# Kernel optimization log

Hardware: AMD Instinct MI355X
Metric: run time of the kernel (lower is better)

## Reference

```python
import jax, jax.numpy as jnp
import numpy as np


def conv2d(x, w, b):
    # x: [B,C,H,W], w: [O,C,K,K] (VALID, stride 1)
    out = jax.lax.conv_general_dilated(
        x, w, window_strides=(1, 1), padding='VALID',
        dimension_numbers=('NCHW', 'OIHW', 'NCHW'))
    return out + b[None, :, None, None]


def deform_conv2d(x, offset, w, b):
    # torchvision DeformConv2d semantics, offset_groups=1, stride=1, padding=0.
    # x: [B,C,H,W]; offset: [B, 2*K*K, Ho, Wo] with (dy, dx) interleaved per tap.
    B, C, H, W = x.shape
    O, _, K, _ = w.shape
    KK = K * K
    Ho, Wo = H - K + 1, W - K + 1
    off = offset.reshape(B, KK, 2, Ho, Wo)
    ky = (jnp.arange(KK) // K).astype(x.dtype)
    kx = (jnp.arange(KK) % K).astype(x.dtype)
    # sampling positions p0 + p_k + dp  -> [B, KK, Ho, Wo]
    py = ky[None, :, None, None] + jnp.arange(Ho, dtype=x.dtype)[None, None, :, None] + off[:, :, 0]
    px = kx[None, :, None, None] + jnp.arange(Wo, dtype=x.dtype)[None, None, None, :] + off[:, :, 1]
    y0 = jnp.floor(py)
    x0 = jnp.floor(px)
    wy = py - y0  # fractional parts
    wx = px - x0
    y0i = y0.astype(jnp.int32)
    x0i = x0.astype(jnp.int32)

    def corner(yi, xi):
        valid = ((yi >= 0) & (yi < H) & (xi >= 0) & (xi < W)).astype(x.dtype)
        yc = jnp.clip(yi, 0, H - 1)
        xc = jnp.clip(xi, 0, W - 1)
        # per-batch gather over all channels -> [B, C, KK, Ho, Wo]
        g = jax.vmap(lambda im, a, bb: im[:, a, bb])(x, yc, xc)
        return g * valid[:, None]

    v00 = corner(y0i, x0i)
    v01 = corner(y0i, x0i + 1)
    v10 = corner(y0i + 1, x0i)
    v11 = corner(y0i + 1, x0i + 1)
    wy_ = wy[:, None]  # [B,1,KK,Ho,Wo]
    wx_ = wx[:, None]
    samp = (v00 * (1 - wy_) * (1 - wx_) + v01 * (1 - wy_) * wx_
            + v10 * wy_ * (1 - wx_) + v11 * wy_ * wx_)
    out = jnp.einsum('bckhw,ock->bohw', samp, w.reshape(O, C, KK))
    return out + b[None, :, None, None]


_STAGES = [
    # (in_ch, out_ch, K)
    (1, 16, 3), (16, 32, 3), (32, 16, 5), (16, 16, 7), (16, 8, 5), (8, 4, 3),
]


def setup_inputs() -> dict:
    key = jax.random.key(0)
    keys = iter(jax.random.split(key, 64))
    inp = {'x': jax.random.normal(next(keys), (512, 1, 33, 33), dtype=jnp.float32)}
    for i, (ci, co, k) in enumerate(_STAGES, start=1):
        # offset-predicting conv: small init so offsets stay near the regular grid
        inp[f'ow{i}'] = jax.random.normal(next(keys), (2 * k * k, ci, k, k), dtype=jnp.float32) * 0.05
        inp[f'ob{i}'] = jax.random.normal(next(keys), (2 * k * k,), dtype=jnp.float32) * 0.05
        scale = 1.0 / np.sqrt(ci * k * k)
        inp[f'w{i}'] = jax.random.normal(next(keys), (co, ci, k, k), dtype=jnp.float32) * scale
        inp[f'b{i}'] = jax.random.normal(next(keys), (co,), dtype=jnp.float32) * scale
    inp['fc1_w'] = jax.random.normal(next(keys), (256, 13 * 13 * 4), dtype=jnp.float32) * (1.0 / np.sqrt(676))
    inp['fc1_b'] = jnp.zeros((256,), dtype=jnp.float32)
    inp['fc2_w'] = jax.random.normal(next(keys), (10, 256), dtype=jnp.float32) * (1.0 / np.sqrt(256))
    inp['fc2_b'] = jnp.zeros((10,), dtype=jnp.float32)
    return inp


def reference(x, ow1, ob1, w1, b1, ow2, ob2, w2, b2, ow3, ob3, w3, b3,
              ow4, ob4, w4, b4, ow5, ob5, w5, b5, ow6, ob6, w6, b6,
              fc1_w, fc1_b, fc2_w, fc2_b):
    h = jax.nn.relu(deform_conv2d(x, conv2d(x, ow1, ob1), w1, b1))
    h = jax.nn.relu(deform_conv2d(h, conv2d(h, ow2, ob2), w2, b2))
    h = deform_conv2d(h, conv2d(h, ow3, ob3), w3, b3)  # NOTE: no ReLU on stage 3 (matches source)
    h = jax.nn.relu(deform_conv2d(h, conv2d(h, ow4, ob4), w4, b4))
    h = jax.nn.relu(deform_conv2d(h, conv2d(h, ow5, ob5), w5, b5))
    h = jax.nn.relu(deform_conv2d(h, conv2d(h, ow6, ob6), w6, b6))
    flat = h.reshape(h.shape[0], -1)  # [B, 4*13*13]
    z = jax.nn.relu(flat @ fc1_w.T + fc1_b)
    return z @ fc2_w.T + fc2_b
```

## Files before the change

kernel.cpp:

```cpp
#include <hip/hip_runtime.h>

typedef __attribute__((ext_vector_type(8))) short bf16x8;
typedef __attribute__((ext_vector_type(4))) float f32x4;
typedef __attribute__((ext_vector_type(4))) unsigned int u32x4;
typedef unsigned short ushort_t;

__device__ inline ushort_t bf16_trunc(float f) { return (ushort_t)(__float_as_uint(f) >> 16); }
__device__ inline float bf16_to_f(ushort_t u) { return __uint_as_float(((unsigned int)u) << 16); }

__device__ inline unsigned int hi_pair(unsigned int u1, unsigned int u0) {
    return __builtin_amdgcn_perm(u1, u0, 0x07060302u);
}

__device__ inline void split8(const f32x4 sA, const f32x4 sB, bf16x8& ahi, bf16x8& alo)
{
    unsigned int u[8], h[8], d[8];
#pragma unroll
    for (int j = 0; j < 4; ++j) {
        u[j]     = __float_as_uint(sA[j]);
        u[4 + j] = __float_as_uint(sB[j]);
    }
#pragma unroll
    for (int j = 0; j < 8; ++j) {
        h[j] = u[j] & 0xffff0000u;
        d[j] = __float_as_uint(__uint_as_float(u[j]) - __uint_as_float(h[j]));
    }
    union { u32x4 w; bf16x8 v; } H, L;
    H.w = (u32x4){hi_pair(h[1], h[0]), hi_pair(h[3], h[2]), hi_pair(h[5], h[4]), hi_pair(h[7], h[6])};
    L.w = (u32x4){hi_pair(d[1], d[0]), hi_pair(d[3], d[2]), hi_pair(d[5], d[4]), hi_pair(d[7], d[6])};
    ahi = H.v;
    alo = L.v;
}

template<int CI, int KK, int KKPAD, int NPAD, int OC>
__global__ __launch_bounds__(256)
void wprep(const float* __restrict__ w, ushort_t* __restrict__ bhi, ushort_t* __restrict__ blo)
{
    const int idx = blockIdx.x * 256 + threadIdx.x;
    if (idx >= KKPAD * NPAD * CI) return;
    const int kk  = idx / (NPAD * CI);
    const int rem = idx - kk * (NPAD * CI);
    const int n   = rem / CI;
    const int ci  = rem - n * CI;
    const float v = (kk < KK && n < OC) ? w[((size_t)n * CI + ci) * KK + kk] : 0.f;
    const ushort_t h = bf16_trunc(v);
    bhi[idx] = h;
    blo[idx] = bf16_trunc(v - bf16_to_f(h));
}

template<int CI, int KK, int TPAD, int NPAD, int OC>
__global__ __launch_bounds__(256)
void wprep_d(const float* __restrict__ w, ushort_t* __restrict__ bhi, ushort_t* __restrict__ blo)
{
    constexpr int NPASS = (CI + 7) / 8;
    constexpr int TOTAL = NPASS * TPAD * NPAD * 8;
    const int idx = blockIdx.x * 256 + threadIdx.x;
    if (idx >= TOTAL) return;
    const int j     = idx & 7;
    const int n     = (idx >> 3) % NPAD;
    const int kslot = (idx >> 3) / NPAD;
    const int pass  = kslot / TPAD;
    const int tap   = kslot - pass * TPAD;
    const int ci    = pass * 8 + j;
    const float v = (tap < KK && n < OC && ci < CI) ? w[((size_t)n * CI + ci) * KK + tap] : 0.f;
    const ushort_t h = bf16_trunc(v);
    bhi[idx] = h;
    blo[idx] = bf16_trunc(v - bf16_to_f(h));
}

template<int CI, int K, int H, int W, int Ho, int Wo, int OC, int NTTOT, int NT0, int KSTEPS>
__global__ __launch_bounds__(256)
void conv_mfma(const ushort_t* __restrict__ Xhi, const ushort_t* __restrict__ Xlo,
               const ushort_t* __restrict__ Bhi, const ushort_t* __restrict__ Blo,
               const float* __restrict__ bias, float* __restrict__ out, int Mtotal)
{
    constexpr int NPAD = NTTOT * 16;
    constexpr int HW   = H * W;
    constexpr int HoWo = Ho * Wo;
    constexpr int NPASS = CI / 8;
    constexpr int TKS  = 32 / CI;
    constexpr int ROWS = TKS * NT0 * 16;
    constexpr int BSTR = CI + 8;
    constexpr int CH8  = CI / 8;
    constexpr int CHUNKS = ROWS * CH8;

    __shared__ __align__(16) ushort_t sBh[2][ROWS * BSTR];
    __shared__ __align__(16) ushort_t sBl[2][ROWS * BSTR];

    const int tid  = threadIdx.x;
    const int lane = tid & 63;
    const int wid  = tid >> 6;
    const int col  = lane & 15;
    const int quad = lane >> 4;

    const int mBase  = blockIdx.x * 256 + wid * 64;
    const int ntBase = blockIdx.y * NT0;

    int aBase[4];
#pragma unroll
    for (int mt = 0; mt < 4; ++mt) {
        int mm = mBase + mt * 16 + col;
        if (mm >= Mtotal) mm = Mtotal - 1;
        const int b   = mm / HoWo;
        const int pos = mm - b * HoWo;
        const int oy  = pos / Wo;
        const int ox  = pos - oy * Wo;
        aBase[mt] = b * NPASS * HW + oy * W + ox;
    }

    f32x4 acc[4][NT0];
#pragma unroll
    for (int mt = 0; mt < 4; ++mt)
#pragma unroll
        for (int nt = 0; nt < NT0; ++nt) acc[mt][nt] = (f32x4){0.f, 0.f, 0.f, 0.f};

    auto loadSlab = [&](int ks, int buf) {
        const int tap0 = ks * TKS;
        for (int i = tid; i < CHUNKS; i += 256) {
            const int row = i / CH8;
            const int c8  = i - row * CH8;
            const int t   = row / (NT0 * 16);
            const int nn  = row - t * (NT0 * 16);
            int n = ntBase * 16 + nn;
            if (n > NPAD - 1) n = NPAD - 1;
            const int g = ((tap0 + t) * NPAD + n) * CI + c8 * 8;
            *(bf16x8*)(sBh[buf] + row * BSTR + c8 * 8) = *(const bf16x8*)(Bhi + g);
            *(bf16x8*)(sBl[buf] + row * BSTR + c8 * 8) = *(const bf16x8*)(Blo + g);
        }
    };

    bf16x8 ah[2][4], al[2][4];

    auto loadA = [&](int ks, int pb) {
        const int k0   = ks * 32 + quad * 8;
        const int tap  = k0 / CI;
        const int ci   = k0 - tap * CI;
        const int g    = ci >> 3;
        const int dkk  = (tap / K) * W + (tap - (tap / K) * K);
#pragma unroll
        for (int mt = 0; mt < 4; ++mt) {
            const size_t aoff = (size_t)(aBase[mt] + g * HW + dkk) * 8;
            ah[pb][mt] = *(const bf16x8*)(Xhi + aoff);
            al[pb][mt] = *(const bf16x8*)(Xlo + aoff);
        }
    };

    loadA(0, 0);
    loadSlab(0, 0);
    __syncthreads();

#pragma unroll
    for (int ks = 0; ks < KSTEPS; ++ks) {
        if (ks + 1 < KSTEPS) {
            loadA(ks + 1, (ks + 1) & 1);
            loadSlab(ks + 1, (ks + 1) & 1);
        }

        const int k0   = ks * 32 + quad * 8;
        const int tap  = k0 / CI;
        const int tloc = tap - ks * TKS;
        const int ci   = k0 - tap * CI;
        const int pb   = ks & 1;

        const ushort_t* __restrict__ bhp = sBh[pb];
        const ushort_t* __restrict__ blp = sBl[pb];
#pragma unroll
        for (int nt = 0; nt < NT0; ++nt) {
            const int ntg = ntBase + nt;
            if (ntg < NTTOT) {
                const int lrow = ((tloc * NT0 + nt) * 16 + col) * BSTR + ci;
                const bf16x8 bh = *(const bf16x8*)(bhp + lrow);
                const bf16x8 bl = *(const bf16x8*)(blp + lrow);
#pragma unroll
                for (int mt = 0; mt < 4; ++mt) {
                    acc[mt][nt] = __builtin_amdgcn_mfma_f32_16x16x32_bf16(ah[pb][mt], bh, acc[mt][nt], 0, 0, 0);
                    acc[mt][nt] = __builtin_amdgcn_mfma_f32_16x16x32_bf16(al[pb][mt], bh, acc[mt][nt], 0, 0, 0);
                    acc[mt][nt] = __builtin_amdgcn_mfma_f32_16x16x32_bf16(ah[pb][mt], bl, acc[mt][nt], 0, 0, 0);
                }
            }
        }
        __syncthreads();
    }

#pragma unroll
    for (int mt = 0; mt < 4; ++mt) {
#pragma unroll
        for (int nt = 0; nt < NT0; ++nt) {
            const int ntg = ntBase + nt;
            const int n   = ntg * 16 + col;
            if (ntg < NTTOT && n < OC) {
                const float bv = bias[n];
#pragma unroll
                for (int r = 0; r < 4; ++r) {
                    const int m = mBase + mt * 16 + quad * 4 + r;
                    if (m < Mtotal) {
                        const int b   = m / HoWo;
                        const int pos = m - b * HoWo;
                        out[((size_t)b * OC + n) * HoWo + pos] = acc[mt][nt][r] + bv;
                    }
                }
            }
        }
    }
}

template<int K, int CI, int CO, int H, int W, int Ho, int Wo, bool RELU,
         int MT, int TPAD, bool OUTPL>
__global__ __launch_bounds__(MT * 64, 4)
void deform_mfma(const ushort_t* __restrict__ Xhi, const ushort_t* __restrict__ Xlo,
                 const float* __restrict__ off,
                 const ushort_t* __restrict__ Bph, const ushort_t* __restrict__ Bpl,
                 const float* __restrict__ bias,
                 float* __restrict__ outF, ushort_t* __restrict__ oHi, ushort_t* __restrict__ oLo)
{
    static_assert(CI % 8 == 0, "channel-grouped layout requires CI % 8 == 0");
    constexpr int KK     = K * K;
    constexpr int HW     = H * W;
    constexpr int HoWo   = Ho * Wo;
    constexpr int GP     = CI / 8;
    constexpr int NPO    = CO / 8;
    constexpr int NT     = (CO + 15) / 16;
    constexpr int NPAD   = NT * 16;
    constexpr int TSTR   = CI + 4;
    constexpr int TG     = TPAD / 4;
    constexpr int nMB    = (HoWo + MT * 16 - 1) / (MT * 16);
    constexpr int THREADS = MT * 64;
    __shared__ __align__(16) float tile[HW * TSTR];

    const int b    = blockIdx.x / nMB;
    const int mb   = blockIdx.x - b * nMB;
    const int tid  = threadIdx.x;
    const int wid  = tid >> 6;
    const int lane = tid & 63;
    const int col  = lane & 15;
    const int quad = lane >> 4;

    const int pixel0 = (mb * MT + wid) * 16;
    const int s      = pixel0 + col;
    const bool am    = (s < HoWo);
    const int oy = s / Wo, ox = s - oy * Wo;

    const float* offB = off + (size_t)b * 2 * KK * HoWo;

    f32x4 acc[NT];
#pragma unroll
    for (int nt = 0; nt < NT; ++nt) acc[nt] = (f32x4){0.f, 0.f, 0.f, 0.f};

    for (int pos = tid; pos < HW; pos += THREADS) {
        float* tp = tile + pos * TSTR;
#pragma unroll
        for (int g = 0; g < GP; ++g) {
            const size_t gbase = ((size_t)(b * GP + g) * HW + pos) * 8;
            const bf16x8 h8 = *(const bf16x8*)(Xhi + gbase);
            const bf16x8 l8 = *(const bf16x8*)(Xlo + gbase);
            f32x4 vA, vB;
#pragma unroll
            for (int j = 0; j < 4; ++j) {
                vA[j] = bf16_to_f((ushort_t)h8[j])     + bf16_to_f((ushort_t)l8[j]);
                vB[j] = bf16_to_f((ushort_t)h8[4 + j]) + bf16_to_f((ushort_t)l8[4 + j]);
            }
            *(f32x4*)(tp + g * 8)     = vA;
            *(f32x4*)(tp + g * 8 + 4) = vB;
        }
    }
    __syncthreads();

#pragma unroll
    for (int tg = 0; tg < TG; ++tg) {
        const int tap = tg * 4 + quad;

        float w00 = 0.f, w01 = 0.f, w10 = 0.f, w11 = 0.f;
        int   i00 = 0,   i01 = 0,   i10 = 0,   i11 = 0;

        if (am && tap < KK) {
            const float dy = offB[(size_t)(2 * tap + 0) * HoWo + s];
            const float dx = offB[(size_t)(2 * tap + 1) * HoWo + s];
            const float py = (float)(tap / K + oy) + dy;
            const float px = (float)(tap % K + ox) + dx;
            const float y0f = floorf(py), x0f = floorf(px);
            const float wy = py - y0f, wx = px - x0f;
            const int y0 = (int)y0f, x0 = (int)x0f;
            const int y1 = y0 + 1,   x1 = x0 + 1;

            const float m00 = (y0 >= 0 && y0 < H && x0 >= 0 && x0 < W) ? 1.f : 0.f;
            const float m01 = (y0 >= 0 && y0 < H && x1 >= 0 && x1 < W) ? 1.f : 0.f;
            const float m10 = (y1 >= 0 && y1 < H && x0 >= 0 && x0 < W) ? 1.f : 0.f;
            const float m11 = (y1 >= 0 && y1 < H && x1 >= 0 && x1 < W) ? 1.f : 0.f;

            w00 = (1.f - wy) * (1.f - wx) * m00;
            w01 = (1.f - wy) * wx         * m01;
            w10 = wy         * (1.f - wx) * m10;
            w11 = wy         * wx         * m11;

            const int y0c = min(max(y0, 0), H - 1), y1c = min(max(y1, 0), H - 1);
            const int x0c = min(max(x0, 0), W - 1), x1c = min(max(x1, 0), W - 1);
            i00 = (y0c * W + x0c) * TSTR;
            i01 = (y0c * W + x1c) * TSTR;
            i10 = (y1c * W + x0c) * TSTR;
            i11 = (y1c * W + x1c) * TSTR;
        }

#pragma unroll
        for (int g = 0; g < GP; ++g) {
            const float* tp = tile + g * 8;
            const f32x4 a00 = *(const f32x4*)(tp + i00);
            const f32x4 c00 = *(const f32x4*)(tp + i00 + 4);
            const f32x4 a01 = *(const f32x4*)(tp + i01);
            const f32x4 c01 = *(const f32x4*)(tp + i01 + 4);
            const f32x4 a10 = *(const f32x4*)(tp + i10);
            const f32x4 c10 = *(const f32x4*)(tp + i10 + 4);
            const f32x4 a11 = *(const f32x4*)(tp + i11);
            const f32x4 c11 = *(const f32x4*)(tp + i11 + 4);

            f32x4 sA = a00 * w00 + a01 * w01 + a10 * w10 + a11 * w11;
            f32x4 sB = c00 * w00 + c01 * w01 + c10 * w10 + c11 * w11;

            bf16x8 ahi, alo;
            split8(sA, sB, ahi, alo);

            const int kslot = g * TPAD + tap;
#pragma unroll
            for (int nt = 0; nt < NT; ++nt) {
                const bf16x8 bh = *(const bf16x8*)(Bph + ((size_t)kslot * NPAD + nt * 16 + col) * 8);
                const bf16x8 bl = *(const bf16x8*)(Bpl + ((size_t)kslot * NPAD + nt * 16 + col) * 8);
                acc[nt] = __builtin_amdgcn_mfma_f32_16x16x32_bf16(ahi, bh, acc[nt], 0, 0, 0);
                acc[nt] = __builtin_amdgcn_mfma_f32_16x16x32_bf16(alo, bh, acc[nt], 0, 0, 0);
                acc[nt] = __builtin_amdgcn_mfma_f32_16x16x32_bf16(ahi, bl, acc[nt], 0, 0, 0);
            }
        }
    }

#pragma unroll
    for (int nt = 0; nt < NT; ++nt) {
        const int n = nt * 16 + col;
        if (n < CO) {
            const float bv = bias[n];
#pragma unroll
            for (int r = 0; r < 4; ++r) {
                const int m = pixel0 + quad * 4 + r;
                if (m < HoWo) {
                    float v = acc[nt][r] + bv;
                    if (RELU) v = fmaxf(v, 0.f);
                    if (OUTPL) {
                        const size_t o = (((size_t)b * NPO + (n >> 3)) * HoWo + m) * 8 + (n & 7);
                        const ushort_t h = bf16_trunc(v);
                        oHi[o] = h;
                        oLo[o] = bf16_trunc(v - bf16_to_f(h));
                    } else {
                        outF[((size_t)b * CO + n) * HoWo + m] = v;
                    }
                }
            }
        }
    }
}

template<int K, int CI, int CO, int H, int W, int Ho, int Wo, bool RELU,
         int CSPLIT, int STRIDE, int THREADS, int SPLIT, bool OUTPL>
__global__ __launch_bounds__(THREADS)
void deform_lds(const float* __restrict__ x, const float* __restrict__ off,
                const float* __restrict__ w, const float* __restrict__ bias,
                float* __restrict__ outF, ushort_t* __restrict__ oHi, ushort_t* __restrict__ oLo)
{
    constexpr int KK    = K * K;
    constexpr int HW    = H * W;
    constexpr int HoWo  = Ho * Wo;
    constexpr int NPASS = CI / CSPLIT;
    constexpr int NPO   = (CO + 7) / 8;
    constexpr int CHUNK = (HoWo + SPLIT - 1) / SPLIT;
    static_assert(CHUNK <= THREADS, "chunk must fit in one block");
    __shared__ __align__(16) float tile[HW * STRIDE];

    const int b   = blockIdx.x / SPLIT;
    const int sp  = blockIdx.x - b * SPLIT;
    const int tid = threadIdx.x;
    const int s   = sp * CHUNK + tid;
    const bool active = (tid < CHUNK) && (s < HoWo);

    const int oy = s / Wo, ox = s - oy * Wo;
    const float* offp = off + ((size_t)b * 2 * KK) * HoWo + s;

    float acc[CO];
#pragma unroll
    for (int o = 0; o < CO; ++o) acc[o] = 0.f;

    for (int pass = 0; pass < NPASS; ++pass) {
        const int cbase = pass * CSPLIT;
        __syncthreads();
        for (int pos = tid; pos < HW; pos += THREADS) {
#pragma unroll
            for (int c = 0; c < CSPLIT; ++c)
                tile[pos * STRIDE + c] = x[((size_t)b * CI + (cbase + c)) * HW + pos];
        }
        __syncthreads();

        if (active) {
            for (int kk = 0; kk < KK; ++kk) {
                const float dy = offp[(size_t)(2 * kk + 0) * HoWo];
                const float dx = offp[(size_t)(2 * kk + 1) * HoWo];
                const float py = (float)(kk / K + oy) + dy;
                const float px = (float)(kk % K + ox) + dx;
                const float y0f = floorf(py), x0f = floorf(px);
                const float wy = py - y0f, wx = px - x0f;
                const int y0 = (int)y0f, x0 = (int)x0f;
                const int y1 = y0 + 1,   x1 = x0 + 1;

                const float m00 = (y0 >= 0 && y0 < H && x0 >= 0 && x0 < W) ? 1.f : 0.f;
                const float m01 = (y0 >= 0 && y0 < H && x1 >= 0 && x1 < W) ? 1.f : 0.f;
                const float m10 = (y1 >= 0 && y1 < H && x0 >= 0 && x0 < W) ? 1.f : 0.f;
                const float m11 = (y1 >= 0 && y1 < H && x1 >= 0 && x1 < W) ? 1.f : 0.f;

                const float w00 = (1.f - wy) * (1.f - wx) * m00;
                const float w01 = (1.f - wy) * wx         * m01;
                const float w10 = wy         * (1.f - wx) * m10;
                const float w11 = wy         * wx         * m11;

                const int y0c = min(max(y0, 0), H - 1), y1c = min(max(y1, 0), H - 1);
                const int x0c = min(max(x0, 0), W - 1), x1c = min(max(x1, 0), W - 1);
                const int i00 = (y0c * W + x0c) * STRIDE;
                const int i01 = (y0c * W + x1c) * STRIDE;
                const int i10 = (y1c * W + x0c) * STRIDE;
                const int i11 = (y1c * W + x1c) * STRIDE;

                if constexpr (CSPLIT % 4 == 0) {
#pragma unroll
                    for (int cg = 0; cg < CSPLIT; cg += 4) {
                        const f32x4 v00 = *(const f32x4*)(tile + i00 + cg);
                        const f32x4 v01 = *(const f32x4*)(tile + i01 + cg);
                        const f32x4 v10 = *(const f32x4*)(tile + i10 + cg);
                        const f32x4 v11 = *(const f32x4*)(tile + i11 + cg);
#pragma unroll
                        for (int j = 0; j < 4; ++j) {
                            const float sv = fmaf(v11[j], w11, fmaf(v10[j], w10,
                                             fmaf(v01[j], w01, v00[j] * w00)));
#pragma unroll
                            for (int o = 0; o < CO; ++o)
                                acc[o] = fmaf(sv, w[(size_t)(o * CI + cbase + cg + j) * KK + kk], acc[o]);
                        }
                    }
                } else {
                    const float sv = fmaf(tile[i11], w11, fmaf(tile[i10], w10,
                                     fmaf(tile[i01], w01, tile[i00] * w00)));
#pragma unroll
                    for (int o = 0; o < CO; ++o)
                        acc[o] = fmaf(sv, w[(size_t)(o * CI + cbase) * KK + kk], acc[o]);
                }
            }
        }
    }

    if (active) {
#pragma unroll
        for (int o = 0; o < CO; ++o) {
            float v = acc[o] + bias[o];
            if (RELU) v = fmaxf(v, 0.f);
            if (OUTPL) {
                const size_t oi = (((size_t)b * NPO + (o >> 3)) * HoWo + s) * 8 + (o & 7);
                const ushort_t h = bf16_trunc(v);
                oHi[oi] = h;
                oLo[oi] = bf16_trunc(v - bf16_to_f(h));
            } else {
                outF[((size_t)b * CO + o) * HoWo + s] = v;
            }
        }
    }
}

template<int K, int CI, int NOC, int OC, int H, int W, int Ho, int Wo, int PIX>
__global__ __launch_bounds__(256)
void conv_tile(const float* __restrict__ x, const float* __restrict__ w,
               const float* __restrict__ bias, float* __restrict__ out)
{
    constexpr int KK   = K * K;
    constexpr int HoWo = Ho * Wo;
    constexpr int WoG  = (Wo + PIX - 1) / PIX;
    constexpr int G    = Ho * WoG;
    constexpr int XV   = PIX + K - 1;

    const int oc0   = blockIdx.y * NOC;
    const int g_all = blockIdx.x * 256 + threadIdx.x;
    const int b     = g_all / G;
    const int g     = g_all - b * G;
    const int oy    = g / WoG;
    const int ox0   = (g - oy * WoG) * PIX;

    const float* xbp = x + (b * CI) * (H * W) + oy * W + ox0;
    const float* wp  = w + oc0 * (CI * KK);

    float acc[PIX][NOC];
#pragma unroll
    for (int p = 0; p < PIX; ++p)
#pragma unroll
        for (int j = 0; j < NOC; ++j) acc[p][j] = bias[oc0 + j];

    const int lim = W - 1 - ox0;

    for (int ci = 0; ci < CI; ++ci) {
        const float* xc = xbp + ci * (H * W);
#pragma unroll
        for (int ky = 0; ky < K; ++ky) {
            float xv[XV];
#pragma unroll
            for (int i = 0; i < XV; ++i) {
                const int off = (i <= lim) ? i : lim;
                xv[i] = xc[ky * W + off];
            }
#pragma unroll
            for (int kx = 0; kx < K; ++kx) {
#pragma unroll
                for (int p = 0; p < PIX; ++p) {
                    const float v = xv[p + kx];
#pragma unroll
                    for (int j = 0; j < NOC; ++j)
                        acc[p][j] = fmaf(v, wp[j * (CI * KK) + ci * KK + ky * K + kx], acc[p][j]);
                }
            }
        }
    }

    float* op = out + (b * OC + oc0) * HoWo + oy * Wo + ox0;
#pragma unroll
    for (int p = 0; p < PIX; ++p) {
        if (ox0 + p < Wo) {
#pragma unroll
            for (int j = 0; j < NOC; ++j) op[j * HoWo + p] = acc[p][j];
        }
    }
}

template<int IN, int OUT>
__global__ __launch_bounds__(256)
void wtrans(const float* __restrict__ w, float* __restrict__ wt)
{
    const int idx = blockIdx.x * 256 + threadIdx.x;
    if (idx >= IN * OUT) return;
    const int i = idx / OUT, j = idx - i * OUT;
    wt[idx] = w[(size_t)j * IN + i];
}

template<int IN, int OUT, bool RELU>
__global__ __launch_bounds__(256)
void fc_t(const float* __restrict__ h, const float* __restrict__ wt,
          const float* __restrict__ bias, float* __restrict__ out, int B)
{
    const int idx = blockIdx.x * 256 + threadIdx.x;
    if (idx >= B * OUT) return;
    const int b = idx / OUT;
    const int j = idx - b * OUT;
    const float* hb = h + (size_t)b * IN;
    float acc = bias[j];
#pragma unroll 4
    for (int i = 0; i < IN; ++i)
        acc = fmaf(hb[i], wt[(size_t)i * OUT + j], acc);
    if (RELU) acc = fmaxf(acc, 0.f);
    out[idx] = acc;
}

extern "C" void kernel_launch(void* const* d_in, const int* in_sizes, int n_in,
                              void* d_out, int out_size, void* d_ws, size_t ws_size,
                              hipStream_t stream)
{
    const int B = 512;
    const float* x = (const float*)d_in[0];
    const float *ow[6], *ob[6], *w[6], *bi[6];
    for (int i = 0; i < 6; ++i) {
        ow[i] = (const float*)d_in[1 + 4 * i];
        ob[i] = (const float*)d_in[2 + 4 * i];
        w[i]  = (const float*)d_in[3 + 4 * i];
        bi[i] = (const float*)d_in[4 + 4 * i];
    }
    const float* fc1w = (const float*)d_in[25];
    const float* fc1b = (const float*)d_in[26];
    const float* fc2w = (const float*)d_in[27];
    const float* fc2b = (const float*)d_in[28];
    float* out = (float*)d_out;

    float* P   = (float*)d_ws;
    float* Q   = P  + 14000000;
    float* OFF = Q  + 14000000;
    float* Z   = OFF + 18200000;
    ushort_t* WBhi = (ushort_t*)(Z + 200000);
    ushort_t* WBlo = WBhi + 200000;
    ushort_t* WDhi = WBlo + 200000;
    ushort_t* WDlo = WDhi + 200000;
    float* WT1 = (float*)(WDlo + 200000);
    float* WT2 = WT1 + 173056;

    const dim3 blk(256);
    #define GRIDT(Ho, Wo, PIX, NG) dim3((B * (Ho) * (((Wo) + (PIX) - 1) / (PIX)) + 255) / 256, (NG), 1)
    #define CEILDIV(a, b) (((a) + (b) - 1) / (b))

    ushort_t* PL2h = (ushort_t*)Q;  ushort_t* PL2l = PL2h + (size_t)(B * 961 + 2048) * 16;
    ushort_t* PL3h = (ushort_t*)P;  ushort_t* PL3l = PL3h + (size_t)(B * 841 + 2048) * 32;
    ushort_t* PL4h = (ushort_t*)Q;  ushort_t* PL4l = PL4h + (size_t)(B * 625 + 2048) * 16;
    ushort_t* PL5h = (ushort_t*)P;  ushort_t* PL5l = PL5h + (size_t)(B * 361 + 2048) * 16;

    conv_tile<3, 1, 6, 18, 33, 33, 31, 31, 4><<<GRIDT(31, 31, 4, 3), blk, 0, stream>>>(x, ow[0], ob[0], OFF);
    deform_lds<3, 1, 16, 33, 33, 31, 31, true, 1, 1, 512, 2, true><<<dim3(B * 2), dim3(512), 0, stream>>>(x, OFF, w[0], bi[0], nullptr, PL2h, PL2l);

    {
        const int Mv = B * 841;
        wprep<16, 9, 10, 32, 18><<<CEILDIV(10 * 32 * 16, 256), blk, 0, stream>>>(ow[1], WBhi, WBlo);
        conv_mfma<16, 3, 31, 31, 29, 29, 18, 2, 2, 5><<<dim3(CEILDIV(Mv, 256), 1), blk, 0, stream>>>(PL2h, PL2l, WBhi, WBlo, ob[1], OFF, Mv);
        wprep_d<16, 9, 12, 32, 32><<<CEILDIV(2 * 12 * 32 * 8, 256), blk, 0, stream>>>(w[1], WDhi, WDlo);
        deform_mfma<3, 16, 32, 31, 31, 29, 29, true, 8, 12, true><<<dim3(B * 7), dim3(512), 0, stream>>>(PL2h, PL2l, OFF, WDhi, WDlo, bi[1], nullptr, PL3h, PL3l);
    }
    {
        const int Mv = B * 625;
        wprep<32, 25, 25, 64, 50><<<CEILDIV(25 * 64 * 32, 256), blk, 0, stream>>>(ow[2], WBhi, WBlo);
        conv_mfma<32, 5, 29, 29, 25, 25, 50, 4, 4, 25><<<dim3(CEILDIV(Mv, 256), 1), blk, 0, stream>>>(PL3h, PL3l, WBhi, WBlo, ob[2], OFF, Mv);
        wprep_d<32, 25, 28, 16, 16><<<CEILDIV(4 * 28 * 16 * 8, 256), blk, 0, stream>>>(w[2], WDhi, WDlo);
        deform_mfma<5, 32, 16, 29, 29, 25, 25, false, 14, 28, true><<<dim3(B * 3), dim3(896), 0, stream>>>(PL3h, PL3l, OFF, WDhi, WDlo, bi[2], nullptr, PL4h, PL4l);
    }
    {
        const int Mv = B * 361;
        wprep<16, 49, 50, 112, 98><<<CEILDIV(50 * 112 * 16, 256), blk, 0, stream>>>(ow[3], WBhi, WBlo);
        conv_mfma<16, 7, 25, 25, 19, 19, 98, 7, 4, 25><<<dim3(CEILDIV(Mv, 256), 2), blk, 0, stream>>>(PL4h, PL4l, WBhi, WBlo, ob[3], OFF, Mv);
        wprep_d<16, 49, 52, 16, 16><<<CEILDIV(2 * 52 * 16 * 8, 256), blk, 0, stream>>>(w[3], WDhi, WDlo);
        deform_mfma<7, 16, 16, 25, 25, 19, 19, true, 8, 52, true><<<dim3(B * 3), dim3(512), 0, stream>>>(PL4h, PL4l, OFF, WDhi, WDlo, bi[3], nullptr, PL5h, PL5l);
    }
    {
        const int Mv = B * 225;
        wprep<16, 25, 26, 64, 50><<<CEILDIV(26 * 64 * 16, 256), blk, 0, stream>>>(ow[4], WBhi, WBlo);
        conv_mfma<16, 5, 19, 19, 15, 15, 50, 4, 4, 13><<<dim3(CEILDIV(Mv, 256), 1), blk, 0, stream>>>(PL5h, PL5l, WBhi, WBlo, ob[4], OFF, Mv);
        wprep_d<16, 25, 28, 16, 8><<<CEILDIV(2 * 28 * 16 * 8, 256), blk, 0, stream>>>(w[4], WDhi, WDlo);
        deform_mfma<5, 16, 8, 19, 19, 15, 15, true, 4, 28, false><<<dim3(B * 4), dim3(256), 0, stream>>>(PL5h, PL5l, OFF, WDhi, WDlo, bi[4], Q, nullptr, nullptr);
    }
    conv_tile<3, 8, 6, 18, 15, 15, 13, 13, 4><<<GRIDT(13, 13, 4, 3), blk, 0, stream>>>(Q, ow[5], ob[5], OFF);
    deform_lds<3, 8, 4, 15, 15, 13, 13, true, 8, 12, 192, 1, false><<<dim3(B), dim3(192), 0, stream>>>(Q, OFF, w[5], bi[5], P, nullptr, nullptr);

    wtrans<676, 256><<<CEILDIV(676 * 256, 256), blk, 0, stream>>>(fc1w, WT1);
    wtrans<256, 10><<<CEILDIV(256 * 10, 256), blk, 0, stream>>>(fc2w, WT2);
    fc_t<676, 256, true><<<dim3(CEILDIV(B * 256, 256)), blk, 0, stream>>>(P, WT1, fc1b, Z, B);
    fc_t<256, 10, false><<<dim3(CEILDIV(B * 10, 256)), blk, 0, stream>>>(Z, WT2, fc2b, out, B);

    #undef GRIDT
    #undef CEILDIV
}
```

Baseline: 817.2 us.

## Use packed FP32 bilinear math, skip empty pixel tiles, enlarge deform blocks

The bilinear interpolation in deform_mfma now uses v_pk_mul_f32/v_pk_fma_f32 inline asm to process two channels per instruction. A guard skips the tap loop for waves whose pixel tile lies entirely outside the output. Three deform_mfma launches are retuned to use more waves per block and fewer blocks, so each block's LDS input tile serves more output pixels. The inline asm may limit compiler scheduling, and larger blocks can lower occupancy.

```diff
diff --git a/kernel.cpp b/kernel.cpp
--- a/kernel.cpp
+++ b/kernel.cpp
@@ -2,11 +2,23 @@
 
 typedef __attribute__((ext_vector_type(8))) short bf16x8;
 typedef __attribute__((ext_vector_type(4))) float f32x4;
+typedef __attribute__((ext_vector_type(2))) float f32x2;
 typedef __attribute__((ext_vector_type(4))) unsigned int u32x4;
 typedef unsigned short ushort_t;
 
 __device__ inline ushort_t bf16_trunc(float f) { return (ushort_t)(__float_as_uint(f) >> 16); }
 __device__ inline float bf16_to_f(ushort_t u) { return __uint_as_float(((unsigned int)u) << 16); }
+
+__device__ inline f32x2 pk_mul(f32x2 a, f32x2 b) {
+    f32x2 d;
+    asm("v_pk_mul_f32 %0, %1, %2" : "=v"(d) : "v"(a), "v"(b));
+    return d;
+}
+__device__ inline f32x2 pk_fma(f32x2 a, f32x2 b, f32x2 c) {
+    f32x2 d;
+    asm("v_pk_fma_f32 %0, %1, %2, %3" : "=v"(d) : "v"(a), "v"(b), "v"(c));
+    return d;
+}
 
 __device__ inline unsigned int hi_pair(unsigned int u1, unsigned int u0) {
     return __builtin_amdgcn_perm(u1, u0, 0x07060302u);
@@ -265,67 +277,92 @@
     }
     __syncthreads();
 
-#pragma unroll
-    for (int tg = 0; tg < TG; ++tg) {
-        const int tap = tg * 4 + quad;
-
-        float w00 = 0.f, w01 = 0.f, w10 = 0.f, w11 = 0.f;
-        int   i00 = 0,   i01 = 0,   i10 = 0,   i11 = 0;
-
-        if (am && tap < KK) {
-            const float dy = offB[(size_t)(2 * tap + 0) * HoWo + s];
-            const float dx = offB[(size_t)(2 * tap + 1) * HoWo + s];
-            const float py = (float)(tap / K + oy) + dy;
-            const float px = (float)(tap % K + ox) + dx;
-            const float y0f = floorf(py), x0f = floorf(px);
-            const float wy = py - y0f, wx = px - x0f;
-            const int y0 = (int)y0f, x0 = (int)x0f;
-            const int y1 = y0 + 1,   x1 = x0 + 1;
-
-            const float m00 = (y0 >= 0 && y0 < H && x0 >= 0 && x0 < W) ? 1.f : 0.f;
-            const float m01 = (y0 >= 0 && y0 < H && x1 >= 0 && x1 < W) ? 1.f : 0.f;
-            const float m10 = (y1 >= 0 && y1 < H && x0 >= 0 && x0 < W) ? 1.f : 0.f;
-            const float m11 = (y1 >= 0 && y1 < H && x1 >= 0 && x1 < W) ? 1.f : 0.f;
-
-            w00 = (1.f - wy) * (1.f - wx) * m00;
-            w01 = (1.f - wy) * wx         * m01;
-            w10 = wy         * (1.f - wx) * m10;
-            w11 = wy         * wx         * m11;
-
-            const int y0c = min(max(y0, 0), H - 1), y1c = min(max(y1, 0), H - 1);
-            const int x0c = min(max(x0, 0), W - 1), x1c = min(max(x1, 0), W - 1);
-            i00 = (y0c * W + x0c) * TSTR;
-            i01 = (y0c * W + x1c) * TSTR;
-            i10 = (y1c * W + x0c) * TSTR;
-            i11 = (y1c * W + x1c) * TSTR;
-        }
-
-#pragma unroll
-        for (int g = 0; g < GP; ++g) {
-            const float* tp = tile + g * 8;
-            const f32x4 a00 = *(const f32x4*)(tp + i00);
-            const f32x4 c00 = *(const f32x4*)(tp + i00 + 4);
-            const f32x4 a01 = *(const f32x4*)(tp + i01);
-            const f32x4 c01 = *(const f32x4*)(tp + i01 + 4);
-            const f32x4 a10 = *(const f32x4*)(tp + i10);
-            const f32x4 c10 = *(const f32x4*)(tp + i10 + 4);
-            const f32x4 a11 = *(const f32x4*)(tp + i11);
-            const f32x4 c11 = *(const f32x4*)(tp + i11 + 4);
-
-            f32x4 sA = a00 * w00 + a01 * w01 + a10 * w10 + a11 * w11;
-            f32x4 sB = c00 * w00 + c01 * w01 + c10 * w10 + c11 * w11;
-
-            bf16x8 ahi, alo;
-            split8(sA, sB, ahi, alo);
-
-            const int kslot = g * TPAD + tap;
-#pragma unroll
-            for (int nt = 0; nt < NT; ++nt) {
-                const bf16x8 bh = *(const bf16x8*)(Bph + ((size_t)kslot * NPAD + nt * 16 + col) * 8);
-                const bf16x8 bl = *(const bf16x8*)(Bpl + ((size_t)kslot * NPAD + nt * 16 + col) * 8);
-                acc[nt] = __builtin_amdgcn_mfma_f32_16x16x32_bf16(ahi, bh, acc[nt], 0, 0, 0);
-                acc[nt] = __builtin_amdgcn_mfma_f32_16x16x32_bf16(alo, bh, acc[nt], 0, 0, 0);
-                acc[nt] = __builtin_amdgcn_mfma_f32_16x16x32_bf16(ahi, bl, acc[nt], 0, 0, 0);
+    if (pixel0 < HoWo) {
+#pragma unroll
+        for (int tg = 0; tg < TG; ++tg) {
+            const int tap = tg * 4 + quad;
+
+            float w00 = 0.f, w01 = 0.f, w10 = 0.f, w11 = 0.f;
+            int   i00 = 0,   i01 = 0,   i10 = 0,   i11 = 0;
+
+            if (am && tap < KK) {
+                const float dy = offB[(size_t)(2 * tap + 0) * HoWo + s];
+                const float dx = offB[(size_t)(2 * tap + 1) * HoWo + s];
+                const float py = (float)(tap / K + oy) + dy;
+                const float px = (float)(tap % K + ox) + dx;
+                const float y0f = floorf(py), x0f = floorf(px);
+                const float wy = py - y0f, wx = px - x0f;
+                const int y0 = (int)y0f, x0 = (int)x0f;
+                const int y1 = y0 + 1,   x1 = x0 + 1;
+
+                const float m00 = (y0 >= 0 && y0 < H && x0 >= 0 && x0 < W) ? 1.f : 0.f;
+                const float m01 = (y0 >= 0 && y0 < H && x1 >= 0 && x1 < W) ? 1.f : 0.f;
+                const float m10 = (y1 >= 0 && y1 < H && x0 >= 0 && x0 < W) ? 1.f : 0.f;
+                const float m11 = (y1 >= 0 && y1 < H && x1 >= 0 && x1 < W) ? 1.f : 0.f;
+
+                w00 = (1.f - wy) * (1.f - wx) * m00;
+                w01 = (1.f - wy) * wx         * m01;
+                w10 = wy         * (1.f - wx) * m10;
+                w11 = wy         * wx         * m11;
+
+                const int y0c = min(max(y0, 0), H - 1), y1c = min(max(y1, 0), H - 1);
+                const int x0c = min(max(x0, 0), W - 1), x1c = min(max(x1, 0), W - 1);
+                i00 = (y0c * W + x0c) * TSTR;
+                i01 = (y0c * W + x1c) * TSTR;
+                i10 = (y1c * W + x0c) * TSTR;
+                i11 = (y1c * W + x1c) * TSTR;
+            }
+
+            const f32x2 w00p = {w00, w00}, w01p = {w01, w01};
+            const f32x2 w10p = {w10, w10}, w11p = {w11, w11};
+
+#pragma unroll
+            for (int g = 0; g < GP; ++g) {
+                const float* tp = tile + g * 8;
+                const f32x4 a00 = *(const f32x4*)(tp + i00);
+                const f32x4 c00 = *(const f32x4*)(tp + i00 + 4);
+                const f32x4 a01 = *(const f32x4*)(tp + i01);
+                const f32x4 c01 = *(const f32x4*)(tp + i01 + 4);
+                const f32x4 a10 = *(const f32x4*)(tp + i10);
+                const f32x4 c10 = *(const f32x4*)(tp + i10 + 4);
+                const f32x4 a11 = *(const f32x4*)(tp + i11);
+                const f32x4 c11 = *(const f32x4*)(tp + i11 + 4);
+
+#define LOH(v) __builtin_shufflevector(v, v, 0, 1)
+#define HIH(v) __builtin_shufflevector(v, v, 2, 3)
+                f32x2 sA0 = pk_mul(LOH(a00), w00p);
+                sA0 = pk_fma(LOH(a01), w01p, sA0);
+                sA0 = pk_fma(LOH(a10), w10p, sA0);
+                sA0 = pk_fma(LOH(a11), w11p, sA0);
+                f32x2 sA1 = pk_mul(HIH(a00), w00p);
+                sA1 = pk_fma(HIH(a01), w01p, sA1);
+                sA1 = pk_fma(HIH(a10), w10p, sA1);
+                sA1 = pk_fma(HIH(a11), w11p, sA1);
+                f32x2 sB0 = pk_mul(LOH(c00), w00p);
+                sB0 = pk_fma(LOH(c01), w01p, sB0);
+                sB0 = pk_fma(LOH(c10), w10p, sB0);
+                sB0 = pk_fma(LOH(c11), w11p, sB0);
+                f32x2 sB1 = pk_mul(HIH(c00), w00p);
+                sB1 = pk_fma(HIH(c01), w01p, sB1);
+                sB1 = pk_fma(HIH(c10), w10p, sB1);
+                sB1 = pk_fma(HIH(c11), w11p, sB1);
+#undef LOH
+#undef HIH
+                const f32x4 sA = __builtin_shufflevector(sA0, sA1, 0, 1, 2, 3);
+                const f32x4 sB = __builtin_shufflevector(sB0, sB1, 0, 1, 2, 3);
+
+                bf16x8 ahi, alo;
+                split8(sA, sB, ahi, alo);
+
+                const int kslot = g * TPAD + tap;
+#pragma unroll
+                for (int nt = 0; nt < NT; ++nt) {
+                    const bf16x8 bh = *(const bf16x8*)(Bph + ((size_t)kslot * NPAD + nt * 16 + col) * 8);
+                    const bf16x8 bl = *(const bf16x8*)(Bpl + ((size_t)kslot * NPAD + nt * 16 + col) * 8);
+                    acc[nt] = __builtin_amdgcn_mfma_f32_16x16x32_bf16(ahi, bh, acc[nt], 0, 0, 0);
+                    acc[nt] = __builtin_amdgcn_mfma_f32_16x16x32_bf16(alo, bh, acc[nt], 0, 0, 0);
+                    acc[nt] = __builtin_amdgcn_mfma_f32_16x16x32_bf16(ahi, bl, acc[nt], 0, 0, 0);
+                }
             }
         }
     }
@@ -603,7 +640,7 @@
         wprep<16, 9, 10, 32, 18><<<CEILDIV(10 * 32 * 16, 256), blk, 0, stream>>>(ow[1], WBhi, WBlo);
         conv_mfma<16, 3, 31, 31, 29, 29, 18, 2, 2, 5><<<dim3(CEILDIV(Mv, 256), 1), blk, 0, stream>>>(PL2h, PL2l, WBhi, WBlo, ob[1], OFF, Mv);
         wprep_d<16, 9, 12, 32, 32><<<CEILDIV(2 * 12 * 32 * 8, 256), blk, 0, stream>>>(w[1], WDhi, WDlo);
-        deform_mfma<3, 16, 32, 31, 31, 29, 29, true, 8, 12, true><<<dim3(B * 7), dim3(512), 0, stream>>>(PL2h, PL2l, OFF, WDhi, WDlo, bi[1], nullptr, PL3h, PL3l);
+        deform_mfma<3, 16, 32, 31, 31, 29, 29, true, 14, 12, true><<<dim3(B * 4), dim3(896), 0, stream>>>(PL2h, PL2l, OFF, WDhi, WDlo, bi[1], nullptr, PL3h, PL3l);
     }
     {
         const int Mv = B * 625;
@@ -617,14 +654,14 @@
         wprep<16, 49, 50, 112, 98><<<CEILDIV(50 * 112 * 16, 256), blk, 0, stream>>>(ow[3], WBhi, WBlo);
         conv_mfma<16, 7, 25, 25, 19, 19, 98, 7, 4, 25><<<dim3(CEILDIV(Mv, 256), 2), blk, 0, stream>>>(PL4h, PL4l, WBhi, WBlo, ob[3], OFF, Mv);
         wprep_d<16, 49, 52, 16, 16><<<CEILDIV(2 * 52 * 16 * 8, 256), blk, 0, stream>>>(w[3], WDhi, WDlo);
-        deform_mfma<7, 16, 16, 25, 25, 19, 19, true, 8, 52, true><<<dim3(B * 3), dim3(512), 0, stream>>>(PL4h, PL4l, OFF, WDhi, WDlo, bi[3], nullptr, PL5h, PL5l);
+        deform_mfma<7, 16, 16, 25, 25, 19, 19, true, 12, 52, true><<<dim3(B * 2), dim3(768), 0, stream>>>(PL4h, PL4l, OFF, WDhi, WDlo, bi[3], nullptr, PL5h, PL5l);
     }
     {
         const int Mv = B * 225;
         wprep<16, 25, 26, 64, 50><<<CEILDIV(26 * 64 * 16, 256), blk, 0, stream>>>(ow[4], WBhi, WBlo);
         conv_mfma<16, 5, 19, 19, 15, 15, 50, 4, 4, 13><<<dim3(CEILDIV(Mv, 256), 1), blk, 0, stream>>>(PL5h, PL5l, WBhi, WBlo, ob[4], OFF, Mv);
         wprep_d<16, 25, 28, 16, 8><<<CEILDIV(2 * 28 * 16 * 8, 256), blk, 0, stream>>>(w[4], WDhi, WDlo);
-        deform_mfma<5, 16, 8, 19, 19, 15, 15, true, 4, 28, false><<<dim3(B * 4), dim3(256), 0, stream>>>(PL5h, PL5l, OFF, WDhi, WDlo, bi[4], Q, nullptr, nullptr);
+        deform_mfma<5, 16, 8, 19, 19, 15, 15, true, 8, 28, false><<<dim3(B * 2), dim3(512), 0, stream>>>(PL5h, PL5l, OFF, WDhi, WDlo, bi[4], Q, nullptr, nullptr);
     }
     conv_tile<3, 8, 6, 18, 15, 15, 13, 13, 4><<<GRIDT(13, 13, 4, 3), blk, 0, stream>>>(Q, ow[5], ob[5], OFF);
     deform_lds<3, 8, 4, 15, 15, 13, 13, true, 8, 12, 192, 1, false><<<dim3(B), dim3(192), 0, stream>>>(Q, OFF, w[5], bi[5], P, nullptr, nullptr);
```

Result: no change. 824.2 us (+0.9%).
